# Optimization experiments

Measured on AMD Instinct MI355X. Metric: run time of the kernel, lower is better.

The kernel has to match this reference:

```python
import jax, jax.numpy as jnp
import numpy as np

EPS = 1e-6
B, CIN, COUT, N, S, M1, M2 = 4, 32, 32, 8192, 8, 12, 12
X, Y = 2 * M1 + 1, 2 * M2 + 1


def setup_inputs() -> dict:
    key = jax.random.key(0)
    ks = jax.random.split(key, 20)
    x = jax.random.normal(ks[0], (B, CIN, N), dtype=jnp.float32)
    loc = jax.random.uniform(ks[1], (B, N, 2), dtype=jnp.float32)
    # per-batch permutation of point indices; equal-size subdomains of N//S points
    ind = jnp.stack([jax.random.permutation(k, N) for k in jax.random.split(ks[2], B)]).astype(jnp.int32)
    ss = 1.0 / S
    sc = 1.0 / (CIN * COUT)
    u = lambda k, shp, s: s * jax.random.uniform(k, shp, dtype=jnp.float32)
    inp = {
        'x': x, 'loc': loc, 'ind': ind,
        'w1s_re': u(ks[3], (S, X, M2), ss), 'w1s_im': u(ks[4], (S, X, M2), ss),
        'w2s_re': u(ks[5], (S, M1 + 1, 1), ss), 'w2s_im': u(ks[6], (S, M1 + 1, 1), ss),
        'w1_re': u(ks[7], (CIN, COUT, X, M2), sc), 'w1_im': u(ks[8], (CIN, COUT, X, M2), sc),
        'w2_re': u(ks[9], (CIN, COUT, M1 + 1, 1), sc), 'w2_im': u(ks[10], (CIN, COUT, M1 + 1, 1), sc),
        'w1sb_re': u(ks[11], (S, X, M2), ss), 'w1sb_im': u(ks[12], (S, X, M2), ss),
        'w2sb_re': u(ks[13], (S, M1 + 1, 1), ss), 'w2sb_im': u(ks[14], (S, M1 + 1, 1), ss),
    }
    return inp


def _forward(x, loc, ind, w1s, w2s, w1, w2, w1sb, w2sb):
    b, cin, n = x.shape
    s, xg_dim, m2 = w1s.shape
    m1 = (xg_dim - 1) // 2
    xx, yy = 2 * m1 + 1, 2 * m2 + 1
    p = n // s
    norm = jnp.asarray(1.0 / np.sqrt(xx * yy), jnp.float32)

    # gather per-subdomain points (equal partitions replace the sep ragged split)
    xg = jnp.take_along_axis(x, ind[:, None, :], axis=2).reshape(b, cin, s, p)
    locg = jnp.take_along_axis(loc, ind[:, :, None], axis=1).reshape(b, s, p, 2)

    # per-subdomain min-max normalization of coords to [-pi, pi]
    om = jnp.swapaxes(locg, -1, -2)                      # [b,s,2,p]
    om = om - om.min(-1, keepdims=True)
    om = om / (om.max(-1, keepdims=True) + EPS)
    om = om * (2.0 * jnp.pi) - jnp.pi

    kx = (jnp.arange(xx) - m1).astype(jnp.float32)
    ky = (jnp.arange(yy) - m2).astype(jnp.float32)
    # exact (type-1) NUDFT basis; conj-wrapped adjoint = sum_p d_p exp(-i k.omega_p)
    E1 = jnp.exp(-1j * om[:, :, 0, :, None] * kx)        # [b,s,p,X]
    E2 = jnp.exp(-1j * om[:, :, 1, :, None] * ky)        # [b,s,p,Y]

    coef = jnp.einsum('bcsp,bspx,bspy->bcsxy', xg.astype(jnp.complex64), E1, E2) * norm

    i1 = coef[..., :m2]                                  # [b,c,s,X,m2]
    i2 = coef[:, :, :, :m1 + 1, m2:m2 + 1]               # [b,c,s,m1+1,1]

    i1 = jnp.einsum('bisxy,sxy->bixy', i1, w1s)
    i2 = jnp.einsum('bisxy,sxy->bixy', i2, w2s)
    i1 = jnp.einsum('bixy,ioxy->boxy', i1, w1)
    i2 = jnp.einsum('bixy,ioxy->boxy', i2, w2)
    i1 = jnp.einsum('boxy,sxy->bosxy', i1, w1sb)
    i2 = jnp.einsum('boxy,sxy->bosxy', i2, w2sb)

    cout = i1.shape[1]
    full = jnp.zeros((b, cout, s, xx, yy), jnp.complex64)
    full = full.at[..., :m2].set(i1)
    full = full.at[..., yy - m2:].set(jnp.conj(i1[..., ::-1, ::-1]))
    full = full.at[..., xx - m1 - 1:, m2:m2 + 1].set(jnp.conj(i2[..., ::-1, ::-1]))
    full = full.at[..., :m1 + 1, m2:m2 + 1].set(i2)      # overwrites center row (mode 0)

    # conj-wrapped forward NUFFT: sum_k c_k exp(+i k.omega_p)
    outc = jnp.einsum('bcsxy,bspx,bspy->bcsp', full, jnp.conj(E1), jnp.conj(E2)) * norm
    outr = outc.real                                     # [b,cout,s,p]

    # per-subdomain min-max renormalization back to input data range
    t = outr - outr.min(-1, keepdims=True)
    t = t / (t.max(-1, keepdims=True) + EPS)
    mn = xg.min(-1, keepdims=True)
    mx = xg.max(-1, keepdims=True)
    vals = t * (mx - mn) + mn                            # needs cin == cout

    # scatter back: output[b,:,ind[b,j]] = vals[b,:,j]
    inv = jnp.argsort(ind, axis=1)
    return jnp.take_along_axis(vals.reshape(b, cout, n), inv[:, None, :], axis=2)


def reference(x, loc, ind, w1s_re, w1s_im, w2s_re, w2s_im, w1_re, w1_im,
              w2_re, w2_im, w1sb_re, w1sb_im, w2sb_re, w2sb_im):
    c = lambda re, im: (re + 1j * im).astype(jnp.complex64)
    return _forward(x, loc, ind, c(w1s_re, w1s_im), c(w2s_re, w2s_im),
                    c(w1_re, w1_im), c(w2_re, w2_im),
                    c(w1sb_re, w1sb_im), c(w2sb_re, w2sb_im))
```

## Files before the change

### kernel.cpp

```cpp
#include <hip/hip_runtime.h>

#define B_ 4
#define C_ 32
#define N_ 8192
#define S_ 8
#define P_ 1024
#define NM_FWD 325
#define NM_INV 313
#define NORM_F 0.04f

#define PI_F 3.14159265358979f
#define TWOPI_F 6.28318530717959f

__device__ __forceinline__ float blk_red(float v, float* red, bool is_min){
  int tid = threadIdx.x;
  red[tid] = v; __syncthreads();
  for (int off = blockDim.x >> 1; off > 0; off >>= 1){
    if (tid < off) red[tid] = is_min ? fminf(red[tid], red[tid+off]) : fmaxf(red[tid], red[tid+off]);
    __syncthreads();
  }
  float r = red[0]; __syncthreads();
  return r;
}

__global__ __launch_bounds__(256) void k_om(const float* __restrict__ loc,
                                            const int* __restrict__ ind,
                                            float* __restrict__ om){
  int b = blockIdx.x >> 3, s = blockIdx.x & 7;
  int tid = threadIdx.x;
  __shared__ float l0[P_], l1[P_];
  __shared__ float red[256];
  const int* indb = ind + b*N_ + s*P_;
  float mn0=1e30f, mx0=-1e30f, mn1=1e30f, mx1=-1e30f;
  for (int p = tid; p < P_; p += 256){
    int n = indb[p];
    float a = loc[(b*N_ + n)*2];
    float c = loc[(b*N_ + n)*2 + 1];
    l0[p] = a; l1[p] = c;
    mn0 = fminf(mn0, a); mx0 = fmaxf(mx0, a);
    mn1 = fminf(mn1, c); mx1 = fmaxf(mx1, c);
  }
  mn0 = blk_red(mn0, red, true);  mx0 = blk_red(mx0, red, false);
  mn1 = blk_red(mn1, red, true);  mx1 = blk_red(mx1, red, false);
  float i0 = TWOPI_F / (mx0 - mn0 + 1e-6f);
  float i1 = TWOPI_F / (mx1 - mn1 + 1e-6f);
  float* om0 = om + ((b*S_ + s)*2)*P_;
  float* om1 = om0 + P_;
  for (int p = tid; p < P_; p += 256){
    om0[p] = (l0[p] - mn0)*i0 - PI_F;
    om1[p] = (l1[p] - mn1)*i1 - PI_F;
  }
}

__global__ __launch_bounds__(512) void k_xg(const float* __restrict__ x,
                                            const int* __restrict__ ind,
                                            float* __restrict__ xg_t,
                                            float* __restrict__ pmm){
  int blk = blockIdx.x;
  int part = blk & 3, bs = blk >> 2;
  int b = bs >> 3, s = bs & 7;
  int t = threadIdx.x;
  int c = t & 31, pl = t >> 5;
  __shared__ int inds[256];
  __shared__ float rmn[8*32], rmx[8*32];
  if (t < 256) inds[t] = ind[b*N_ + s*P_ + part*256 + t];
  __syncthreads();
  const float* xr = x + (b*C_ + c)*N_;
  float mn = 1e30f, mx = -1e30f;
  int pbase = part*256;
  #pragma unroll 4
  for (int k = 0; k < 16; ++k){
    int pp = pl + k*16;
    float v = xr[inds[pp]];
    xg_t[(bs*P_ + pbase + pp)*C_ + c] = v;
    mn = fminf(mn, v); mx = fmaxf(mx, v);
  }
  mn = fminf(mn, __shfl_xor(mn, 32));
  mx = fmaxf(mx, __shfl_xor(mx, 32));
  int wid = t >> 6;
  if ((t & 63) < 32){ rmn[wid*32 + c] = mn; rmx[wid*32 + c] = mx; }
  __syncthreads();
  if (t < 32){
    float m0 = rmn[t], M0 = rmx[t];
    #pragma unroll
    for (int w = 1; w < 8; ++w){ m0 = fminf(m0, rmn[w*32+t]); M0 = fmaxf(M0, rmx[w*32+t]); }
    pmm[((bs*4 + part)*32 + t)*2]     = m0;
    pmm[((bs*4 + part)*32 + t)*2 + 1] = M0;
  }
}

__global__ __launch_bounds__(256) void k_wt(
    const float* __restrict__ w1s_re, const float* __restrict__ w1s_im,
    const float* __restrict__ w2s_re, const float* __restrict__ w2s_im,
    const float* __restrict__ w1_re,  const float* __restrict__ w1_im,
    const float* __restrict__ w2_re,  const float* __restrict__ w2_im,
    const float* __restrict__ w1sb_re,const float* __restrict__ w1sb_im,
    const float* __restrict__ w2sb_re,const float* __restrict__ w2sb_im,
    float* __restrict__ w1t, float* __restrict__ w1st, float* __restrict__ w1sbt){
  int q = blockIdx.x;
  int t = threadIdx.x;
  bool p1 = (q < 300);
  int x = p1 ? q % 25 : q - 300;
  int y = p1 ? q / 25 : 12;
  for (int idx = t; idx < 1024; idx += 256){
    float wre, wim;
    if (p1){ int wi = (idx*25 + x)*12 + y; wre = w1_re[wi]; wim = w1_im[wi]; }
    else   { int wi = idx*13 + x;          wre = w2_re[wi]; wim = w2_im[wi]; }
    w1t[(size_t)(q*1024 + idx)*2]     = wre;
    w1t[(size_t)(q*1024 + idx)*2 + 1] = wim;
  }
  if (t < 8){
    int s = t;
    float a, b2, c2, d2;
    if (p1){ int wi = (s*25+x)*12+y; a=w1s_re[wi]; b2=w1s_im[wi]; c2=w1sb_re[wi]; d2=w1sb_im[wi]; }
    else   { int wi = s*13+x;        a=w2s_re[wi]; b2=w2s_im[wi]; c2=w2sb_re[wi]; d2=w2sb_im[wi]; }
    w1st[(q*8+s)*2]   = a;  w1st[(q*8+s)*2+1]  = b2;
    w1sbt[(q*8+s)*2]  = c2; w1sbt[(q*8+s)*2+1] = d2;
  }
}

__global__ __launch_bounds__(448) void k_fwd(const float* __restrict__ om,
                                             const float* __restrict__ xg_t,
                                             float* __restrict__ coef_part){
  int blk = blockIdx.x;
  int part = blk & 1;
  int tile = (blk >> 1) % 6;
  int bs   = blk / 12;
  int t = threadIdx.x;
  int ml = t >> 3;
  int q  = t & 7;
  int mf = tile*56 + ml;
  int mfc = min(mf, NM_FWD-1);
  int xo = mfc / 13, yo = mfc - xo*13;
  float kx = (float)(xo - 12), ky = (float)(yo - 12);
  __shared__ float o0s[512], o1s[512];
  __shared__ __align__(16) float xgs[64*32];
  __shared__ float Wre[56*68], Wim[56*68];
  const float* om0 = om + bs*2*P_;
  const float* om1 = om0 + P_;
  for (int i = t; i < 512; i += 448){
    o0s[i] = om0[part*512 + i];
    o1s[i] = om1[part*512 + i];
  }
  float ar[4] = {0,0,0,0}, ai[4] = {0,0,0,0};
  for (int ch = 0; ch < 8; ++ch){
    int pbase = part*512 + ch*64;
    __syncthreads();
    for (int i = t; i < 512; i += 448){
      ((float4*)xgs)[i] = ((const float4*)xg_t)[(bs*P_ + pbase + (i>>3))*8 + (i&7)];
    }
    {
      int ps = t & 7;
      #pragma unroll
      for (int k = 0; k < 8; ++k){
        int p = ps + k*8;
        float th = o0s[ch*64 + p]*kx + o1s[ch*64 + p]*ky;
        float sn, cs; __sincosf(th, &sn, &cs);
        Wre[ml*68 + p] = cs;
        Wim[ml*68 + p] = sn;
      }
    }
    __syncthreads();
    #pragma unroll 8
    for (int p = 0; p < 64; ++p){
      float4 g4 = *(const float4*)&xgs[p*32 + q*4];
      float wre = Wre[ml*68 + p], wim = Wim[ml*68 + p];
      ar[0] += g4.x*wre; ai[0] += g4.x*wim;
      ar[1] += g4.y*wre; ai[1] += g4.y*wim;
      ar[2] += g4.z*wre; ai[2] += g4.z*wim;
      ar[3] += g4.w*wre; ai[3] += g4.w*wim;
    }
  }
  if (mf < NM_FWD){
    float* dst = coef_part + (size_t)((part*32 + bs)*NM_FWD + mf)*64 + q*8;
    #pragma unroll
    for (int j = 0; j < 4; ++j){
      dst[j*2]     = ar[j]*NORM_F;
      dst[j*2 + 1] = -ai[j]*NORM_F;
    }
  }
}

__global__ __launch_bounds__(64) void k_mid(const float* __restrict__ coef_part,
    const float* __restrict__ w1t, const float* __restrict__ w1st,
    const float* __restrict__ w1sbt, float* __restrict__ zbuf){
  int blk = blockIdx.x;
  int b = blk / NM_INV, q = blk - b*NM_INV;
  int lane = threadIdx.x;
  int o = lane & 31;
  int hi = lane >> 5;
  bool p1 = (q < 300);
  int x = p1 ? q % 25 : q - 300;
  int y = p1 ? q / 25 : 12;
  int mf = x*13 + y;
  __shared__ float iv[64];
  float are = 0.f, aim = 0.f;
  #pragma unroll
  for (int s = 0; s < 8; ++s){
    const float* cp = coef_part + (size_t)((hi*32 + b*8 + s)*NM_FWD + mf)*64 + o*2;
    float cre = cp[0], cim = cp[1];
    float wre = w1st[(q*8+s)*2], wim = w1st[(q*8+s)*2+1];
    are += cre*wre - cim*wim;
    aim += cre*wim + cim*wre;
  }
  are += __shfl_xor(are, 32);
  aim += __shfl_xor(aim, 32);
  if (hi == 0){ iv[o*2] = are; iv[o*2+1] = aim; }
  __syncthreads();
  float ore = 0.f, oim = 0.f;
  #pragma unroll
  for (int ii = 0; ii < 16; ++ii){
    int i = hi*16 + ii;
    float zre = iv[i*2], zim = iv[i*2+1];
    const float* wp = w1t + (size_t)(q*1024 + i*32 + o)*2;
    float wre = wp[0], wim = wp[1];
    ore += zre*wre - zim*wim;
    oim += zre*wim + zim*wre;
  }
  ore += __shfl_xor(ore, 32);
  oim += __shfl_xor(oim, 32);
  float scale = p1 ? 0.08f : ((x==12) ? 0.04f : 0.08f);
  #pragma unroll
  for (int si = 0; si < 4; ++si){
    int s = hi*4 + si;
    float wre = w1sbt[(q*8+s)*2], wim = w1sbt[(q*8+s)*2+1];
    float zre = (ore*wre - oim*wim)*scale;
    float zim = (ore*wim + oim*wre)*scale;
    size_t oi = (size_t)((b*8 + s)*NM_INV + q)*64 + o*2;
    zbuf[oi] = zre; zbuf[oi+1] = zim;
  }
}

__global__ __launch_bounds__(256) void k_inv(const float* __restrict__ om,
                                             const float* __restrict__ zbuf,
                                             float* __restrict__ routc){
  int blk = blockIdx.x;
  int pt = blk & 15, bs = blk >> 4;
  int p0 = pt*64;
  int t = threadIdx.x;
  int oq = t >> 6, pl = t & 63;
  __shared__ __align__(16) float Zs[64*64];
  const float* zb = zbuf + (size_t)bs*NM_INV*64;
  float o0 = om[bs*2*P_ + p0 + pl];
  float o1 = om[bs*2*P_ + P_ + p0 + pl];
  float d0s, d0c; __sincosf(o0, &d0s, &d0c);
  float d1s, d1c; __sincosf(o1, &d1s, &d1c);
  float rs0, rc0; __sincosf(12.f*(o0+o1), &rs0, &rc0);
  float rre = rc0, rim = -rs0;
  float fre = rre, fim = rim;
  int rowc = 0;
  float acc[8] = {0,0,0,0,0,0,0,0};
  for (int chv = 0; chv < 5; ++chv){
    int m0 = chv*64;
    int mcount = min(64, NM_INV - m0);
    __syncthreads();
    for (int i = t*4; i < mcount*64; i += 1024)
      *(float4*)&Zs[i] = *(const float4*)&zb[m0*64 + i];
    __syncthreads();
    const float* zrow = Zs + oq*16;
    for (int m = 0; m < mcount; ++m){
      if (rowc == 25){
        float nr = rre*d1c - rim*d1s;
        float ni = rre*d1s + rim*d1c;
        rre = nr; rim = ni;
        fre = rre; fim = rim;
        rowc = 0;
      }
      float4 za = *(const float4*)&zrow[m*64];
      float4 zb4 = *(const float4*)&zrow[m*64 + 4];
      float4 zc = *(const float4*)&zrow[m*64 + 8];
      float4 zd = *(const float4*)&zrow[m*64 + 12];
      acc[0] += za.x*fre  - za.y*fim;
      acc[1] += za.z*fre  - za.w*fim;
      acc[2] += zb4.x*fre - zb4.y*fim;
      acc[3] += zb4.z*fre - zb4.w*fim;
      acc[4] += zc.x*fre  - zc.y*fim;
      acc[5] += zc.z*fre  - zc.w*fim;
      acc[6] += zd.x*fre  - zd.y*fim;
      acc[7] += zd.z*fre  - zd.w*fim;
      float nf = fre*d0c - fim*d0s;
      float ni = fre*d0s + fim*d0c;
      fre = nf; fim = ni;
      ++rowc;
    }
  }
  float* outp = routc + (size_t)(bs*C_ + oq*8)*P_ + p0 + pl;
  #pragma unroll
  for (int j = 0; j < 8; ++j)
    outp[(size_t)j*P_] = acc[j];
}

__global__ __launch_bounds__(256) void k_fin(const float* __restrict__ routc,
                                             const float* __restrict__ pmm,
                                             const int* __restrict__ ind,
                                             float* __restrict__ out){
  int blk = blockIdx.x;
  int o = blk & 31, s = (blk >> 5) & 7, b = blk >> 8;
  int bs = b*8 + s;
  int t = threadIdx.x;
  __shared__ float red[256];
  const float* rr = routc + (size_t)(bs*C_ + o)*P_;
  float v[4]; float mn = 1e30f, mx = -1e30f;
  #pragma unroll
  for (int k = 0; k < 4; ++k){
    v[k] = rr[t + k*256];
    mn = fminf(mn, v[k]); mx = fmaxf(mx, v[k]);
  }
  mn = blk_red(mn, red, true);
  mx = blk_red(mx, red, false);
  float xmn = 1e30f, xmx = -1e30f;
  #pragma unroll
  for (int part = 0; part < 4; ++part){
    xmn = fminf(xmn, pmm[((bs*4+part)*32 + o)*2]);
    xmx = fmaxf(xmx, pmm[((bs*4+part)*32 + o)*2 + 1]);
  }
  float scale = (xmx - xmn) / (mx - mn + 1e-6f);
  const int* indb = ind + b*N_ + s*P_;
  float* outb = out + (size_t)(b*C_ + o)*N_;
  #pragma unroll
  for (int k = 0; k < 4; ++k){
    int p = t + k*256;
    outb[indb[p]] = (v[k] - mn)*scale + xmn;
  }
}

extern "C" void kernel_launch(void* const* d_in, const int* in_sizes, int n_in,
                              void* d_out, int out_size, void* d_ws, size_t ws_size,
                              hipStream_t stream){
  const float* x      = (const float*)d_in[0];
  const float* loc    = (const float*)d_in[1];
  const int*   ind    = (const int*)  d_in[2];
  const float* w1s_re = (const float*)d_in[3];
  const float* w1s_im = (const float*)d_in[4];
  const float* w2s_re = (const float*)d_in[5];
  const float* w2s_im = (const float*)d_in[6];
  const float* w1_re  = (const float*)d_in[7];
  const float* w1_im  = (const float*)d_in[8];
  const float* w2_re  = (const float*)d_in[9];
  const float* w2_im  = (const float*)d_in[10];
  const float* w1sb_re= (const float*)d_in[11];
  const float* w1sb_im= (const float*)d_in[12];
  const float* w2sb_re= (const float*)d_in[13];
  const float* w2sb_im= (const float*)d_in[14];
  float* out = (float*)d_out;

  float* ws = (float*)d_ws;
  float* om        = ws;
  float* xg_t      = om + 65536;
  float* pmm       = xg_t + 1048576;
  float* coef_part = pmm + 8192;
  float* zbuf      = coef_part + 1331200;
  float* w1t       = zbuf + 641024;
  float* w1st      = w1t + 641024;
  float* w1sbt     = w1st + 5008;
  float* routc     = xg_t;

  k_om <<<32,   256, 0, stream>>>(loc, ind, om);
  k_xg <<<128,  512, 0, stream>>>(x, ind, xg_t, pmm);
  k_wt <<<NM_INV, 256, 0, stream>>>(w1s_re, w1s_im, w2s_re, w2s_im,
                                    w1_re, w1_im, w2_re, w2_im,
                                    w1sb_re, w1sb_im, w2sb_re, w2sb_im,
                                    w1t, w1st, w1sbt);
  k_fwd<<<384,  448, 0, stream>>>(om, xg_t, coef_part);
  k_mid<<<4*NM_INV, 64, 0, stream>>>(coef_part, w1t, w1st, w1sbt, zbuf);
  k_inv<<<512,  256, 0, stream>>>(om, zbuf, routc);
  k_fin<<<1024, 256, 0, stream>>>(routc, pmm, ind, out);
}
```

Before: 209.6 us.

## Restructure forward NUDFT to per-thread modes with register accumulators, drop LDS staging in inverse

The forward transform now assigns one mode per lane with 32 channel accumulators held in registers. Each thread computes its own sincos per point and reads xg directly from global/cache, replacing the shared-memory W tile and chunked syncs. Partial sums are reduced across two waves through LDS and written into four point-partition buffers, which k_mid sums over. The inverse kernel drops LDS staging of zbuf in favour of direct wave-uniform float4 loads, with an explicit y/x loop structure instead of the row counter branch. The risks are high register pressure (64 accumulators), more sincos evaluations, and a larger intermediate buffer.

```diff
diff --git a/kernel.cpp b/kernel.cpp
--- a/kernel.cpp
+++ b/kernel.cpp
@@ -6,6 +6,7 @@
 #define S_ 8
 #define P_ 1024
 #define NM_FWD 325
+#define NM_PAD 384
 #define NM_INV 313
 #define NORM_F 0.04f
 
@@ -119,69 +120,65 @@
   }
 }
 
-__global__ __launch_bounds__(448) void k_fwd(const float* __restrict__ om,
+__global__ __launch_bounds__(128) void k_fwd(const float* __restrict__ om,
                                              const float* __restrict__ xg_t,
-                                             float* __restrict__ coef_part){
-  int blk = blockIdx.x;
-  int part = blk & 1;
-  int tile = (blk >> 1) % 6;
-  int bs   = blk / 12;
-  int t = threadIdx.x;
-  int ml = t >> 3;
-  int q  = t & 7;
-  int mf = tile*56 + ml;
-  int mfc = min(mf, NM_FWD-1);
-  int xo = mfc / 13, yo = mfc - xo*13;
+                                             float* __restrict__ coef_pair){
+  int blk = blockIdx.x;
+  int ppair = blk & 3;
+  int mw    = (blk >> 2) % 6;
+  int bs    = blk / 24;
+  int t = threadIdx.x;
+  int w = t >> 6;
+  int lane = t & 63;
+  int m = mw*64 + lane;
+  int mc = min(m, NM_FWD-1);
+  int xo = mc / 13, yo = mc - xo*13;
   float kx = (float)(xo - 12), ky = (float)(yo - 12);
-  __shared__ float o0s[512], o1s[512];
-  __shared__ __align__(16) float xgs[64*32];
-  __shared__ float Wre[56*68], Wim[56*68];
-  const float* om0 = om + bs*2*P_;
+  int part = ppair*2 + w;
+  int pbase = part*128;
+  const float* om0 = om + bs*2*P_ + pbase;
   const float* om1 = om0 + P_;
-  for (int i = t; i < 512; i += 448){
-    o0s[i] = om0[part*512 + i];
-    o1s[i] = om1[part*512 + i];
-  }
-  float ar[4] = {0,0,0,0}, ai[4] = {0,0,0,0};
-  for (int ch = 0; ch < 8; ++ch){
-    int pbase = part*512 + ch*64;
-    __syncthreads();
-    for (int i = t; i < 512; i += 448){
-      ((float4*)xgs)[i] = ((const float4*)xg_t)[(bs*P_ + pbase + (i>>3))*8 + (i&7)];
-    }
-    {
-      int ps = t & 7;
-      #pragma unroll
-      for (int k = 0; k < 8; ++k){
-        int p = ps + k*8;
-        float th = o0s[ch*64 + p]*kx + o1s[ch*64 + p]*ky;
-        float sn, cs; __sincosf(th, &sn, &cs);
-        Wre[ml*68 + p] = cs;
-        Wim[ml*68 + p] = sn;
-      }
-    }
-    __syncthreads();
-    #pragma unroll 8
-    for (int p = 0; p < 64; ++p){
-      float4 g4 = *(const float4*)&xgs[p*32 + q*4];
-      float wre = Wre[ml*68 + p], wim = Wim[ml*68 + p];
-      ar[0] += g4.x*wre; ai[0] += g4.x*wim;
-      ar[1] += g4.y*wre; ai[1] += g4.y*wim;
-      ar[2] += g4.z*wre; ai[2] += g4.z*wim;
-      ar[3] += g4.w*wre; ai[3] += g4.w*wim;
-    }
-  }
-  if (mf < NM_FWD){
-    float* dst = coef_part + (size_t)((part*32 + bs)*NM_FWD + mf)*64 + q*8;
-    #pragma unroll
-    for (int j = 0; j < 4; ++j){
-      dst[j*2]     = ar[j]*NORM_F;
-      dst[j*2 + 1] = -ai[j]*NORM_F;
-    }
-  }
-}
-
-__global__ __launch_bounds__(64) void k_mid(const float* __restrict__ coef_part,
+  const float4* xgw = (const float4*)(xg_t + ((size_t)bs*P_ + pbase)*C_);
+  float ar[32], ai[32];
+  #pragma unroll
+  for (int c = 0; c < 32; ++c){ ar[c] = 0.f; ai[c] = 0.f; }
+  for (int p = 0; p < 128; ++p){
+    float o0 = om0[p], o1 = om1[p];
+    float th = o0*kx + o1*ky;
+    float sn, cs; __sincosf(th, &sn, &cs);
+    const float4* xp = xgw + p*8;
+    #pragma unroll
+    for (int cq = 0; cq < 8; ++cq){
+      float4 g = xp[cq];
+      ar[cq*4+0] += g.x*cs; ai[cq*4+0] += g.x*sn;
+      ar[cq*4+1] += g.y*cs; ai[cq*4+1] += g.y*sn;
+      ar[cq*4+2] += g.z*cs; ai[cq*4+2] += g.z*sn;
+      ar[cq*4+3] += g.w*cs; ai[cq*4+3] += g.w*sn;
+    }
+  }
+  __shared__ float redbuf[64*66];
+  if (w == 1){
+    #pragma unroll
+    for (int c = 0; c < 32; ++c){
+      redbuf[lane*66 + c*2]     = ar[c];
+      redbuf[lane*66 + c*2 + 1] = ai[c];
+    }
+  }
+  __syncthreads();
+  if (w == 0 && m < NM_FWD){
+    float* dst = coef_pair + (size_t)((ppair*32 + bs)*NM_PAD + m)*64;
+    #pragma unroll
+    for (int c = 0; c < 16; ++c){
+      float re0 =  (ar[c*2]   + redbuf[lane*66 + c*4])     * NORM_F;
+      float im0 = -(ai[c*2]   + redbuf[lane*66 + c*4 + 1]) * NORM_F;
+      float re1 =  (ar[c*2+1] + redbuf[lane*66 + c*4 + 2]) * NORM_F;
+      float im1 = -(ai[c*2+1] + redbuf[lane*66 + c*4 + 3]) * NORM_F;
+      *(float4*)&dst[c*4] = make_float4(re0, im0, re1, im1);
+    }
+  }
+}
+
+__global__ __launch_bounds__(64) void k_mid(const float* __restrict__ coef_pair,
     const float* __restrict__ w1t, const float* __restrict__ w1st,
     const float* __restrict__ w1sbt, float* __restrict__ zbuf){
   int blk = blockIdx.x;
@@ -196,12 +193,16 @@
   __shared__ float iv[64];
   float are = 0.f, aim = 0.f;
   #pragma unroll
-  for (int s = 0; s < 8; ++s){
-    const float* cp = coef_part + (size_t)((hi*32 + b*8 + s)*NM_FWD + mf)*64 + o*2;
-    float cre = cp[0], cim = cp[1];
-    float wre = w1st[(q*8+s)*2], wim = w1st[(q*8+s)*2+1];
-    are += cre*wre - cim*wim;
-    aim += cre*wim + cim*wre;
+  for (int ppl = 0; ppl < 2; ++ppl){
+    int pp = hi*2 + ppl;
+    #pragma unroll
+    for (int s = 0; s < 8; ++s){
+      const float* cp = coef_pair + (size_t)((pp*32 + b*8 + s)*NM_PAD + mf)*64 + o*2;
+      float cre = cp[0], cim = cp[1];
+      float wre = w1st[(q*8+s)*2], wim = w1st[(q*8+s)*2+1];
+      are += cre*wre - cim*wim;
+      aim += cre*wim + cim*wre;
+    }
   }
   are += __shfl_xor(are, 32);
   aim += __shfl_xor(aim, 32);
@@ -238,38 +239,23 @@
   int pt = blk & 15, bs = blk >> 4;
   int p0 = pt*64;
   int t = threadIdx.x;
-  int oq = t >> 6, pl = t & 63;
-  __shared__ __align__(16) float Zs[64*64];
-  const float* zb = zbuf + (size_t)bs*NM_INV*64;
+  int oq = __builtin_amdgcn_readfirstlane(t >> 6);
+  int pl = t & 63;
+  const float4* zw = (const float4*)(zbuf + (size_t)bs*NM_INV*64 + oq*16);
   float o0 = om[bs*2*P_ + p0 + pl];
   float o1 = om[bs*2*P_ + P_ + p0 + pl];
   float d0s, d0c; __sincosf(o0, &d0s, &d0c);
   float d1s, d1c; __sincosf(o1, &d1s, &d1c);
   float rs0, rc0; __sincosf(12.f*(o0+o1), &rs0, &rc0);
   float rre = rc0, rim = -rs0;
-  float fre = rre, fim = rim;
-  int rowc = 0;
   float acc[8] = {0,0,0,0,0,0,0,0};
-  for (int chv = 0; chv < 5; ++chv){
-    int m0 = chv*64;
-    int mcount = min(64, NM_INV - m0);
-    __syncthreads();
-    for (int i = t*4; i < mcount*64; i += 1024)
-      *(float4*)&Zs[i] = *(const float4*)&zb[m0*64 + i];
-    __syncthreads();
-    const float* zrow = Zs + oq*16;
-    for (int m = 0; m < mcount; ++m){
-      if (rowc == 25){
-        float nr = rre*d1c - rim*d1s;
-        float ni = rre*d1s + rim*d1c;
-        rre = nr; rim = ni;
-        fre = rre; fim = rim;
-        rowc = 0;
-      }
-      float4 za = *(const float4*)&zrow[m*64];
-      float4 zb4 = *(const float4*)&zrow[m*64 + 4];
-      float4 zc = *(const float4*)&zrow[m*64 + 8];
-      float4 zd = *(const float4*)&zrow[m*64 + 12];
+  #pragma unroll 1
+  for (int y = 0; y < 12; ++y){
+    float fre = rre, fim = rim;
+    #pragma unroll 5
+    for (int x = 0; x < 25; ++x){
+      const float4* zp = zw + (size_t)(y*25 + x)*16;
+      float4 za = zp[0], zb4 = zp[1], zc = zp[2], zd = zp[3];
       acc[0] += za.x*fre  - za.y*fim;
       acc[1] += za.z*fre  - za.w*fim;
       acc[2] += zb4.x*fre - zb4.y*fim;
@@ -281,7 +267,28 @@
       float nf = fre*d0c - fim*d0s;
       float ni = fre*d0s + fim*d0c;
       fre = nf; fim = ni;
-      ++rowc;
+    }
+    float nr = rre*d1c - rim*d1s;
+    float ni2 = rre*d1s + rim*d1c;
+    rre = nr; rim = ni2;
+  }
+  {
+    float fre = rre, fim = rim;
+    #pragma unroll 13
+    for (int x = 0; x < 13; ++x){
+      const float4* zp = zw + (size_t)(300 + x)*16;
+      float4 za = zp[0], zb4 = zp[1], zc = zp[2], zd = zp[3];
+      acc[0] += za.x*fre  - za.y*fim;
+      acc[1] += za.z*fre  - za.w*fim;
+      acc[2] += zb4.x*fre - zb4.y*fim;
+      acc[3] += zb4.z*fre - zb4.w*fim;
+      acc[4] += zc.x*fre  - zc.y*fim;
+      acc[5] += zc.z*fre  - zc.w*fim;
+      acc[6] += zd.x*fre  - zd.y*fim;
+      acc[7] += zd.z*fre  - zd.w*fim;
+      float nf = fre*d0c - fim*d0s;
+      float ni = fre*d0s + fim*d0c;
+      fre = nf; fim = ni;
     }
   }
   float* outp = routc + (size_t)(bs*C_ + oq*8)*P_ + p0 + pl;
@@ -348,8 +355,8 @@
   float* om        = ws;
   float* xg_t      = om + 65536;
   float* pmm       = xg_t + 1048576;
-  float* coef_part = pmm + 8192;
-  float* zbuf      = coef_part + 1331200;
+  float* coef_pair = pmm + 8192;
+  float* zbuf      = coef_pair + 3145728;
   float* w1t       = zbuf + 641024;
   float* w1st      = w1t + 641024;
   float* w1sbt     = w1st + 5008;
@@ -361,8 +368,8 @@
                                     w1_re, w1_im, w2_re, w2_im,
                                     w1sb_re, w1sb_im, w2sb_re, w2sb_im,
                                     w1t, w1st, w1sbt);
-  k_fwd<<<384,  448, 0, stream>>>(om, xg_t, coef_part);
-  k_mid<<<4*NM_INV, 64, 0, stream>>>(coef_part, w1t, w1st, w1sbt, zbuf);
+  k_fwd<<<768,  128, 0, stream>>>(om, xg_t, coef_pair);
+  k_mid<<<4*NM_INV, 64, 0, stream>>>(coef_pair, w1t, w1st, w1sbt, zbuf);
   k_inv<<<512,  256, 0, stream>>>(om, zbuf, routc);
   k_fin<<<1024, 256, 0, stream>>>(routc, pmm, ind, out);
 }
```

New measurement: 301.2 us. +43.7%, slower.
